# Kernel optimization log

Hardware: AMD Instinct MI355X
Metric: run time of the kernel (lower is better)

## Reference

```python
import jax, jax.numpy as jnp
import numpy as np

B, S, H, DH = 32, 512, 16, 64  # batch, seq_len (== dim_k), heads, head dim
DM = H * DH                     # d_model = 1024
DK = S                          # Linformer projection dim == seq_len (forced by Linear(dim_k, dim_k))


def setup_inputs() -> dict:
    key = jax.random.key(0)
    ks = jax.random.split(key, 16)
    sc = lambda fan_in: 1.0 / np.sqrt(fan_in)
    inp = {
        "query": jax.random.normal(ks[0], (B, S, DH), jnp.float32),
        "key":   jax.random.normal(ks[1], (B, S, DH), jnp.float32),
        "value": jax.random.normal(ks[2], (B, S, DH), jnp.float32),
        # per-head Q/K/V projections: torch Linear weight [out, in]
        "Wq": jax.random.uniform(ks[3], (H, DH, DH), jnp.float32, -sc(DH), sc(DH)),
        "bq": jax.random.uniform(ks[4], (H, DH), jnp.float32, -sc(DH), sc(DH)),
        "Wk": jax.random.uniform(ks[5], (H, DH, DH), jnp.float32, -sc(DH), sc(DH)),
        "bk": jax.random.uniform(ks[6], (H, DH), jnp.float32, -sc(DH), sc(DH)),
        "Wv": jax.random.uniform(ks[7], (H, DH, DH), jnp.float32, -sc(DH), sc(DH)),
        "bv": jax.random.uniform(ks[8], (H, DH), jnp.float32, -sc(DH), sc(DH)),
        # shared (headwise) E/F projections along the sequence dim: Linear(dim_k, dim_k)
        "E_w": jax.random.uniform(ks[9],  (DK, DK), jnp.float32, -sc(DK), sc(DK)),
        "E_b": jax.random.uniform(ks[10], (DK,),    jnp.float32, -sc(DK), sc(DK)),
        "F_w": jax.random.uniform(ks[11], (DK, DK), jnp.float32, -sc(DK), sc(DK)),
        "F_b": jax.random.uniform(ks[12], (DK,),    jnp.float32, -sc(DK), sc(DK)),
        # output projection Linear(d_model, d_model)
        "out_w": jax.random.uniform(ks[13], (DM, DM), jnp.float32, -sc(DM), sc(DM)),
        "out_b": jax.random.uniform(ks[14], (DM,),    jnp.float32, -sc(DM), sc(DM)),
    }
    return inp


def reference(query, key, value, Wq, bq, Wk, bk, Wv, bv, E_w, E_b, F_w, F_b, out_w, out_b):
    # Per-head linear projections (torch Linear: x @ W.T + b), vectorized over heads
    Q = jnp.einsum('bsd,hed->bhse', query, Wq) + bq[None, :, None, :]   # [B,H,S,DH]
    K = jnp.einsum('bsd,hed->bhse', key,   Wk) + bk[None, :, None, :]
    V = jnp.einsum('bsd,hed->bhse', value, Wv) + bv[None, :, None, :]

    # E projection along seq dim: K.permute -> [B,H,DH,S]; Linear(S,S) -> [B,H,DH,T]
    KE = jnp.einsum('bhsd,ts->bhdt', K, E_w) + E_b[None, None, None, :]  # [B,H,DH,T]
    # F projection along seq dim, then permute back: [B,H,T,DH]
    VF = jnp.einsum('bhsd,ts->bhtd', V, F_w) + F_b[None, None, :, None]  # [B,H,T,DH]

    scale = 1.0 / jnp.sqrt(jnp.float32(DH))  # scale uses d_head (K.size(-1) pre-permute)
    scores = jnp.einsum('bhsd,bhdt->bhst', Q, KE) * scale                # [B,H,S,T]
    attn = jax.nn.softmax(scores, axis=-1)                               # [B,H,S,T]
    head_out = jnp.einsum('bhst,bhtd->bhsd', attn, VF)                   # [B,H,S,DH]

    # concat heads on last dim: [B,S,H*DH]
    mha = head_out.transpose(0, 2, 1, 3).reshape(B, S, DM)
    mha_out = mha @ out_w.T + out_b                                      # [B,S,DM]
    return mha_out, attn
```

## Files before the change

kernel.cpp:

```cpp
#include <hip/hip_runtime.h>
#include <math.h>

#define B_  32
#define S_  512
#define H_  16
#define DH_ 64
#define DM_ 1024
#define T_  512

#define NBHSD (B_*H_*S_*DH_)
#define OFF_ATTN ((size_t)B_*S_*DM_)

__global__ __launch_bounds__(256)
void qkv_proj_kernel(const float* __restrict__ q_in, const float* __restrict__ k_in,
                     const float* __restrict__ v_in,
                     const float* __restrict__ Wq, const float* __restrict__ bq,
                     const float* __restrict__ Wk, const float* __restrict__ bk,
                     const float* __restrict__ Wv, const float* __restrict__ bv,
                     float* __restrict__ Qo, float* __restrict__ Ko, float* __restrict__ Vo)
{
    const int stile = blockIdx.x;
    const int h     = blockIdx.y;
    const int which = blockIdx.z / B_;
    const int b     = blockIdx.z % B_;

    const float* xin; const float* W; const float* bias; float* out;
    if (which == 0)      { xin = q_in; W = Wq; bias = bq; out = Qo; }
    else if (which == 1) { xin = k_in; W = Wk; bias = bk; out = Ko; }
    else                 { xin = v_in; W = Wv; bias = bv; out = Vo; }

    __shared__ float sA[32*68];
    __shared__ float sW[32*68];

    const int tid = threadIdx.x;
    const int dg = tid & 15;
    const int tg = tid >> 4;
    const int s0 = stile * 64;

    float acc[4][4];
    #pragma unroll
    for (int i=0;i<4;i++)
        #pragma unroll
        for (int j=0;j<4;j++) acc[i][j]=0.f;

    for (int dc = 0; dc < 64; dc += 32) {
        __syncthreads();
        for (int idx = tid; idx < 64*32; idx += 256) {
            int s = idx >> 5, d = idx & 31;
            sA[d*68 + s] = xin[((size_t)b*S_ + s0 + s)*DH_ + dc + d];
        }
        for (int idx = tid; idx < 64*32; idx += 256) {
            int e = idx >> 5, d = idx & 31;
            sW[d*68 + e] = W[(size_t)h*DH_*DH_ + (size_t)e*DH_ + dc + d];
        }
        __syncthreads();
        #pragma unroll
        for (int kk = 0; kk < 32; kk++) {
            const float4 a4 = *(const float4*)&sA[kk*68 + tg*4];
            const float4 w4 = *(const float4*)&sW[kk*68 + dg*4];
            const float a[4] = {a4.x,a4.y,a4.z,a4.w};
            const float w[4] = {w4.x,w4.y,w4.z,w4.w};
            #pragma unroll
            for (int i=0;i<4;i++)
                #pragma unroll
                for (int j=0;j<4;j++)
                    acc[i][j] = fmaf(a[i], w[j], acc[i][j]);
        }
    }

    const float4 bv4 = *(const float4*)&bias[h*DH_ + dg*4];
    const float bb[4] = {bv4.x,bv4.y,bv4.z,bv4.w};
    #pragma unroll
    for (int i=0;i<4;i++) {
        int s = s0 + tg*4 + i;
        float4 o;
        o.x = acc[i][0]+bb[0]; o.y = acc[i][1]+bb[1];
        o.z = acc[i][2]+bb[2]; o.w = acc[i][3]+bb[3];
        *(float4*)&out[(((size_t)b*H_ + h)*S_ + s)*DH_ + dg*4] = o;
    }
}

__global__ __launch_bounds__(256)
void gemm128x64_kernel(const float* __restrict__ A, long a_bh_stride, int K,
                       const float* __restrict__ X, long x_bh_stride,
                       const float* __restrict__ bias,
                       float* __restrict__ Y, long y_b_stride, long y_h_stride,
                       int y_row_stride)
{
    const int mtile = blockIdx.x;
    const int bh    = blockIdx.y;

    const float* Ab = A + (long)bh * a_bh_stride + (long)mtile*128*K;
    const float* Xb = X + (long)bh * x_bh_stride;

    __shared__ float sA[32*132];
    __shared__ float sX[32*72];

    const int tid = threadIdx.x;
    const int mg = tid >> 3;
    const int dg = tid & 7;
    const int mg4 = mg << 2;
    const int dg4 = dg << 2;

    float acc[4][8];
    #pragma unroll
    for (int i=0;i<4;i++)
        #pragma unroll
        for (int j=0;j<8;j++) acc[i][j]=0.f;

    for (int kc = 0; kc < K; kc += 32) {
        __syncthreads();
        #pragma unroll
        for (int w = 0; w < 4; w++) {
            int idx = tid + w*256;
            int m = idx >> 3, k4 = idx & 7;
            float4 v = *(const float4*)&Ab[(long)m*K + kc + k4*4];
            int col = (((m >> 2) ^ k4) << 2) + (m & 3);
            sA[(k4*4+0)*132 + col] = v.x;
            sA[(k4*4+1)*132 + col] = v.y;
            sA[(k4*4+2)*132 + col] = v.z;
            sA[(k4*4+3)*132 + col] = v.w;
        }
        #pragma unroll
        for (int w = 0; w < 2; w++) {
            int idx = tid + w*256;
            int k = idx >> 4, d4 = idx & 15;
            *(float4*)&sX[k*72 + d4*4] = *(const float4*)&Xb[(long)(kc+k)*64 + d4*4];
        }
        __syncthreads();
        #pragma unroll
        for (int kk = 0; kk < 32; kk++) {
            const int sm = mg4 ^ ((kk >> 2) << 2);
            const float4 a4 = *(const float4*)&sA[kk*132 + sm];
            const float4 x0 = *(const float4*)&sX[kk*72 + dg4];
            const float4 x1 = *(const float4*)&sX[kk*72 + 32 + dg4];
            const float a[4] = {a4.x,a4.y,a4.z,a4.w};
            const float x[8] = {x0.x,x0.y,x0.z,x0.w,x1.x,x1.y,x1.z,x1.w};
            #pragma unroll
            for (int i=0;i<4;i++)
                #pragma unroll
                for (int j=0;j<8;j++)
                    acc[i][j] = fmaf(a[i], x[j], acc[i][j]);
        }
    }

    const long ybase = (long)(bh >> 4)*y_b_stride + (long)(bh & 15)*y_h_stride
                     + (long)mtile*128*y_row_stride;
    #pragma unroll
    for (int i=0;i<4;i++) {
        int m = mg4 + i;
        float bval = bias ? bias[mtile*128 + m] : 0.f;
        float4 o0, o1;
        o0.x = acc[i][0]+bval; o0.y = acc[i][1]+bval;
        o0.z = acc[i][2]+bval; o0.w = acc[i][3]+bval;
        o1.x = acc[i][4]+bval; o1.y = acc[i][5]+bval;
        o1.z = acc[i][6]+bval; o1.w = acc[i][7]+bval;
        *(float4*)&Y[ybase + (long)m*y_row_stride + dg4]      = o0;
        *(float4*)&Y[ybase + (long)m*y_row_stride + 32 + dg4] = o1;
    }
}

__global__ __launch_bounds__(256)
void attn_softmax_kernel(const float* __restrict__ Q, const float* __restrict__ KEt,
                         float* __restrict__ attnOut)
{
    const int stile = blockIdx.x;
    const int bh    = blockIdx.y;

    __shared__ float sQt[64*36];
    __shared__ float sKt[64*132];

    const int tid = threadIdx.x;
    const int sq  = tid >> 5;
    const int tq  = tid & 31;
    const int tq4 = tq << 2;
    const int s0  = stile * 32;

    #pragma unroll
    for (int w = 0; w < 2; w++) {
        int idx = tid + w*256;
        int s = idx >> 4, d4 = idx & 15;
        float4 v = *(const float4*)&Q[((size_t)bh*S_ + s0 + s)*DH_ + d4*4];
        sQt[(d4*4+0)*36 + s] = v.x * 0.125f;
        sQt[(d4*4+1)*36 + s] = v.y * 0.125f;
        sQt[(d4*4+2)*36 + s] = v.z * 0.125f;
        sQt[(d4*4+3)*36 + s] = v.w * 0.125f;
    }

    float p[4][4][4];

    #pragma unroll
    for (int c = 0; c < 4; c++) {
        __syncthreads();
        #pragma unroll
        for (int w = 0; w < 8; w++) {
            int idx = tid + w*256;
            int t = idx >> 4, d4 = idx & 15;
            float4 v = *(const float4*)&KEt[((size_t)bh*T_ + c*128 + t)*DH_ + d4*4];
            int col = (((t >> 2) ^ d4) << 2) + (t & 3);
            sKt[(d4*4+0)*132 + col] = v.x;
            sKt[(d4*4+1)*132 + col] = v.y;
            sKt[(d4*4+2)*132 + col] = v.z;
            sKt[(d4*4+3)*132 + col] = v.w;
        }
        __syncthreads();

        #pragma unroll
        for (int i=0;i<4;i++)
            #pragma unroll
            for (int j=0;j<4;j++) p[c][i][j] = 0.f;

        #pragma unroll
        for (int kk = 0; kk < 64; kk++) {
            const float4 q4 = *(const float4*)&sQt[kk*36 + sq*4];
            const int st = tq4 ^ ((kk >> 2) << 2);
            const float4 k4 = *(const float4*)&sKt[kk*132 + st];
            const float q[4] = {q4.x,q4.y,q4.z,q4.w};
            const float k[4] = {k4.x,k4.y,k4.z,k4.w};
            #pragma unroll
            for (int i=0;i<4;i++)
                #pragma unroll
                for (int j=0;j<4;j++)
                    p[c][i][j] = fmaf(q[i], k[j], p[c][i][j]);
        }
    }

    #pragma unroll
    for (int i = 0; i < 4; i++) {
        float m = -INFINITY;
        #pragma unroll
        for (int c = 0; c < 4; c++)
            #pragma unroll
            for (int j = 0; j < 4; j++) m = fmaxf(m, p[c][i][j]);
        #pragma unroll
        for (int off = 16; off >= 1; off >>= 1) m = fmaxf(m, __shfl_xor(m, off));

        float sum = 0.f;
        #pragma unroll
        for (int c = 0; c < 4; c++)
            #pragma unroll
            for (int j = 0; j < 4; j++) {
                p[c][i][j] = __expf(p[c][i][j] - m);
                sum += p[c][i][j];
            }
        #pragma unroll
        for (int off = 16; off >= 1; off >>= 1) sum += __shfl_xor(sum, off);
        const float inv = 1.f / sum;

        const size_t rowbase = ((size_t)bh*S_ + s0 + sq*4 + i)*T_;
        #pragma unroll
        for (int c = 0; c < 4; c++) {
            float4 o;
            o.x = p[c][i][0]*inv; o.y = p[c][i][1]*inv;
            o.z = p[c][i][2]*inv; o.w = p[c][i][3]*inv;
            *(float4*)&attnOut[rowbase + c*128 + tq4] = o;
        }
    }
}

__global__ __launch_bounds__(256)
void outproj_kernel(const float* __restrict__ MHA, const float* __restrict__ Wout,
                    const float* __restrict__ bout, float* __restrict__ Yout)
{
    const int i0 = blockIdx.x*128;
    const int n0 = blockIdx.y*128;

    __shared__ float sA[32*132];
    __shared__ float sW[32*132];

    const int tid = threadIdx.x;
    const int mg = tid >> 4;
    const int ng = tid & 15;
    const int mg4 = mg << 2;
    const int ng4 = ng << 2;

    float acc[8][8];
    #pragma unroll
    for (int i=0;i<8;i++)
        #pragma unroll
        for (int j=0;j<8;j++) acc[i][j]=0.f;

    for (int kc = 0; kc < DM_; kc += 32) {
        __syncthreads();
        #pragma unroll
        for (int w = 0; w < 4; w++) {
            int idx = tid + w*256;
            int m = idx >> 3, k4 = idx & 7;
            float4 v = *(const float4*)&MHA[(long)(i0 + m)*DM_ + kc + k4*4];
            int col = (((m >> 2) ^ k4) << 2) + (m & 3);
            sA[(k4*4+0)*132 + col] = v.x;
            sA[(k4*4+1)*132 + col] = v.y;
            sA[(k4*4+2)*132 + col] = v.z;
            sA[(k4*4+3)*132 + col] = v.w;
        }
        #pragma unroll
        for (int w = 0; w < 4; w++) {
            int idx = tid + w*256;
            int n = idx >> 3, k4 = idx & 7;
            float4 v = *(const float4*)&Wout[(long)(n0 + n)*DM_ + kc + k4*4];
            int col = (((n >> 2) ^ k4) << 2) + (n & 3);
            sW[(k4*4+0)*132 + col] = v.x;
            sW[(k4*4+1)*132 + col] = v.y;
            sW[(k4*4+2)*132 + col] = v.z;
            sW[(k4*4+3)*132 + col] = v.w;
        }
        __syncthreads();
        #pragma unroll
        for (int kk = 0; kk < 32; kk++) {
            const int c4 = (kk >> 2) << 2;
            const int sm = mg4 ^ c4;
            const int sn = ng4 ^ c4;
            const float4 a0 = *(const float4*)&sA[kk*132 + sm];
            const float4 a1 = *(const float4*)&sA[kk*132 + 64 + sm];
            const float4 b0 = *(const float4*)&sW[kk*132 + sn];
            const float4 b1 = *(const float4*)&sW[kk*132 + 64 + sn];
            const float a[8] = {a0.x,a0.y,a0.z,a0.w,a1.x,a1.y,a1.z,a1.w};
            const float b[8] = {b0.x,b0.y,b0.z,b0.w,b1.x,b1.y,b1.z,b1.w};
            #pragma unroll
            for (int i=0;i<8;i++)
                #pragma unroll
                for (int j=0;j<8;j++)
                    acc[i][j] = fmaf(a[i], b[j], acc[i][j]);
        }
    }

    const float4 bv0 = *(const float4*)&bout[n0 + ng4];
    const float4 bv1 = *(const float4*)&bout[n0 + 64 + ng4];
    const float bb[8] = {bv0.x,bv0.y,bv0.z,bv0.w,bv1.x,bv1.y,bv1.z,bv1.w};
    #pragma unroll
    for (int ih = 0; ih < 2; ih++)
        #pragma unroll
        for (int ii = 0; ii < 4; ii++) {
            const int ai = ih*4 + ii;
            const long row = (long)(i0 + ih*64 + mg4 + ii)*DM_ + n0;
            float4 o0, o1;
            o0.x = acc[ai][0]+bb[0]; o0.y = acc[ai][1]+bb[1];
            o0.z = acc[ai][2]+bb[2]; o0.w = acc[ai][3]+bb[3];
            o1.x = acc[ai][4]+bb[4]; o1.y = acc[ai][5]+bb[5];
            o1.z = acc[ai][6]+bb[6]; o1.w = acc[ai][7]+bb[7];
            *(float4*)&Yout[row + ng4]      = o0;
            *(float4*)&Yout[row + 64 + ng4] = o1;
        }
}

extern "C" void kernel_launch(void* const* d_in, const int* in_sizes, int n_in,
                              void* d_out, int out_size, void* d_ws, size_t ws_size,
                              hipStream_t stream)
{
    const float* query = (const float*)d_in[0];
    const float* key   = (const float*)d_in[1];
    const float* value = (const float*)d_in[2];
    const float* Wq    = (const float*)d_in[3];
    const float* bq    = (const float*)d_in[4];
    const float* Wk    = (const float*)d_in[5];
    const float* bk    = (const float*)d_in[6];
    const float* Wv    = (const float*)d_in[7];
    const float* bv    = (const float*)d_in[8];
    const float* E_w   = (const float*)d_in[9];
    const float* E_b   = (const float*)d_in[10];
    const float* F_w   = (const float*)d_in[11];
    const float* F_b   = (const float*)d_in[12];
    const float* out_w = (const float*)d_in[13];
    const float* out_b = (const float*)d_in[14];

    float* ws   = (float*)d_ws;
    float* Qb   = ws;
    float* Kb   = ws + (size_t)NBHSD;
    float* Vb   = ws + (size_t)2*NBHSD;
    float* KEt  = ws + (size_t)3*NBHSD;
    float* VF   = ws + (size_t)4*NBHSD;
    float* MHA  = Qb;

    float* mha_out = (float*)d_out;
    float* attn    = (float*)d_out + OFF_ATTN;

    qkv_proj_kernel<<<dim3(S_/64, H_, 3*B_), 256, 0, stream>>>(
        query, key, value, Wq, bq, Wk, bk, Wv, bv, Qb, Kb, Vb);

    gemm128x64_kernel<<<dim3(T_/128, B_*H_), 256, 0, stream>>>(
        E_w, 0, S_, Kb, (long)S_*DH_, E_b,
        KEt, (long)H_*T_*DH_, (long)T_*DH_, DH_);
    gemm128x64_kernel<<<dim3(T_/128, B_*H_), 256, 0, stream>>>(
        F_w, 0, S_, Vb, (long)S_*DH_, F_b,
        VF, (long)H_*T_*DH_, (long)T_*DH_, DH_);

    attn_softmax_kernel<<<dim3(S_/32, B_*H_), 256, 0, stream>>>(Qb, KEt, attn);

    gemm128x64_kernel<<<dim3(S_/128, B_*H_), 256, 0, stream>>>(
        attn, (long)S_*T_, T_, VF, (long)T_*DH_, nullptr,
        MHA, (long)S_*DM_, (long)DH_, DM_);

    outproj_kernel<<<dim3(B_*S_/128, DM_/128), 256, 0, stream>>>(
        MHA, out_w, out_b, mha_out);
}
```

Baseline: 2.114 ms.

## Run output projection on bf16 MFMA with hi/lo split-precision operands

```diff
diff --git a/kernel.cpp b/kernel.cpp
--- a/kernel.cpp
+++ b/kernel.cpp
@@ -10,6 +10,19 @@
 
 #define NBHSD (B_*H_*S_*DH_)
 #define OFF_ATTN ((size_t)B_*S_*DM_)
+
+typedef __attribute__((ext_vector_type(8))) short     bf16x8;
+typedef __attribute__((ext_vector_type(4))) float     f32x4;
+typedef __attribute__((ext_vector_type(8))) unsigned short u16x8;
+
+__device__ __forceinline__ unsigned short f2bf(float x) {
+    unsigned int u = __float_as_uint(x);
+    u = (u + 0x7FFFu + ((u >> 16) & 1u)) >> 16;
+    return (unsigned short)u;
+}
+__device__ __forceinline__ float bf2f(unsigned short h) {
+    return __uint_as_float(((unsigned int)h) << 16);
+}
 
 __global__ __launch_bounds__(256)
 void qkv_proj_kernel(const float* __restrict__ q_in, const float* __restrict__ k_in,
@@ -259,34 +272,37 @@
 }
 
 __global__ __launch_bounds__(256)
-void outproj_kernel(const float* __restrict__ MHA, const float* __restrict__ Wout,
-                    const float* __restrict__ bout, float* __restrict__ Yout)
-{
-    const int i0 = blockIdx.x*128;
-    const int n0 = blockIdx.y*128;
+void pv_bf16out_kernel(const float* __restrict__ A, const float* __restrict__ X,
+                       ushort* __restrict__ Yhi, ushort* __restrict__ Ylo)
+{
+    const int mtile = blockIdx.x;
+    const int bh    = blockIdx.y;
+
+    const float* Ab = A + (size_t)bh*S_*T_ + (size_t)mtile*128*T_;
+    const float* Xb = X + (size_t)bh*T_*DH_;
 
     __shared__ float sA[32*132];
-    __shared__ float sW[32*132];
+    __shared__ float sX[32*72];
 
     const int tid = threadIdx.x;
-    const int mg = tid >> 4;
-    const int ng = tid & 15;
+    const int mg = tid >> 3;
+    const int dg = tid & 7;
     const int mg4 = mg << 2;
-    const int ng4 = ng << 2;
-
-    float acc[8][8];
-    #pragma unroll
-    for (int i=0;i<8;i++)
+    const int dg4 = dg << 2;
+
+    float acc[4][8];
+    #pragma unroll
+    for (int i=0;i<4;i++)
         #pragma unroll
         for (int j=0;j<8;j++) acc[i][j]=0.f;
 
-    for (int kc = 0; kc < DM_; kc += 32) {
+    for (int kc = 0; kc < T_; kc += 32) {
         __syncthreads();
         #pragma unroll
         for (int w = 0; w < 4; w++) {
             int idx = tid + w*256;
             int m = idx >> 3, k4 = idx & 7;
-            float4 v = *(const float4*)&MHA[(long)(i0 + m)*DM_ + kc + k4*4];
+            float4 v = *(const float4*)&Ab[(long)m*T_ + kc + k4*4];
             int col = (((m >> 2) ^ k4) << 2) + (m & 3);
             sA[(k4*4+0)*132 + col] = v.x;
             sA[(k4*4+1)*132 + col] = v.y;
@@ -294,53 +310,151 @@
             sA[(k4*4+3)*132 + col] = v.w;
         }
         #pragma unroll
-        for (int w = 0; w < 4; w++) {
+        for (int w = 0; w < 2; w++) {
             int idx = tid + w*256;
-            int n = idx >> 3, k4 = idx & 7;
-            float4 v = *(const float4*)&Wout[(long)(n0 + n)*DM_ + kc + k4*4];
-            int col = (((n >> 2) ^ k4) << 2) + (n & 3);
-            sW[(k4*4+0)*132 + col] = v.x;
-            sW[(k4*4+1)*132 + col] = v.y;
-            sW[(k4*4+2)*132 + col] = v.z;
-            sW[(k4*4+3)*132 + col] = v.w;
+            int k = idx >> 4, d4 = idx & 15;
+            *(float4*)&sX[k*72 + d4*4] = *(const float4*)&Xb[(long)(kc+k)*64 + d4*4];
         }
         __syncthreads();
         #pragma unroll
         for (int kk = 0; kk < 32; kk++) {
-            const int c4 = (kk >> 2) << 2;
-            const int sm = mg4 ^ c4;
-            const int sn = ng4 ^ c4;
-            const float4 a0 = *(const float4*)&sA[kk*132 + sm];
-            const float4 a1 = *(const float4*)&sA[kk*132 + 64 + sm];
-            const float4 b0 = *(const float4*)&sW[kk*132 + sn];
-            const float4 b1 = *(const float4*)&sW[kk*132 + 64 + sn];
-            const float a[8] = {a0.x,a0.y,a0.z,a0.w,a1.x,a1.y,a1.z,a1.w};
-            const float b[8] = {b0.x,b0.y,b0.z,b0.w,b1.x,b1.y,b1.z,b1.w};
-            #pragma unroll
-            for (int i=0;i<8;i++)
+            const int sm = mg4 ^ ((kk >> 2) << 2);
+            const float4 a4 = *(const float4*)&sA[kk*132 + sm];
+            const float4 x0 = *(const float4*)&sX[kk*72 + dg4];
+            const float4 x1 = *(const float4*)&sX[kk*72 + 32 + dg4];
+            const float a[4] = {a4.x,a4.y,a4.z,a4.w};
+            const float x[8] = {x0.x,x0.y,x0.z,x0.w,x1.x,x1.y,x1.z,x1.w};
+            #pragma unroll
+            for (int i=0;i<4;i++)
                 #pragma unroll
                 for (int j=0;j<8;j++)
-                    acc[i][j] = fmaf(a[i], b[j], acc[i][j]);
-        }
-    }
-
-    const float4 bv0 = *(const float4*)&bout[n0 + ng4];
-    const float4 bv1 = *(const float4*)&bout[n0 + 64 + ng4];
-    const float bb[8] = {bv0.x,bv0.y,bv0.z,bv0.w,bv1.x,bv1.y,bv1.z,bv1.w};
-    #pragma unroll
-    for (int ih = 0; ih < 2; ih++)
-        #pragma unroll
-        for (int ii = 0; ii < 4; ii++) {
-            const int ai = ih*4 + ii;
-            const long row = (long)(i0 + ih*64 + mg4 + ii)*DM_ + n0;
-            float4 o0, o1;
-            o0.x = acc[ai][0]+bb[0]; o0.y = acc[ai][1]+bb[1];
-            o0.z = acc[ai][2]+bb[2]; o0.w = acc[ai][3]+bb[3];
-            o1.x = acc[ai][4]+bb[4]; o1.y = acc[ai][5]+bb[5];
-            o1.z = acc[ai][6]+bb[6]; o1.w = acc[ai][7]+bb[7];
-            *(float4*)&Yout[row + ng4]      = o0;
-            *(float4*)&Yout[row + 64 + ng4] = o1;
-        }
+                    acc[i][j] = fmaf(a[i], x[j], acc[i][j]);
+        }
+    }
+
+    const size_t ybase = (size_t)(bh >> 4)*S_*DM_ + (size_t)(bh & 15)*DH_
+                       + (size_t)mtile*128*DM_;
+    #pragma unroll
+    for (int i=0;i<4;i++) {
+        const int m = mg4 + i;
+        const size_t rb = ybase + (size_t)m*DM_;
+        ushort4 h0, l0, h1, l1;
+        h0.x = f2bf(acc[i][0]); l0.x = f2bf(acc[i][0] - bf2f(h0.x));
+        h0.y = f2bf(acc[i][1]); l0.y = f2bf(acc[i][1] - bf2f(h0.y));
+        h0.z = f2bf(acc[i][2]); l0.z = f2bf(acc[i][2] - bf2f(h0.z));
+        h0.w = f2bf(acc[i][3]); l0.w = f2bf(acc[i][3] - bf2f(h0.w));
+        h1.x = f2bf(acc[i][4]); l1.x = f2bf(acc[i][4] - bf2f(h1.x));
+        h1.y = f2bf(acc[i][5]); l1.y = f2bf(acc[i][5] - bf2f(h1.y));
+        h1.z = f2bf(acc[i][6]); l1.z = f2bf(acc[i][6] - bf2f(h1.z));
+        h1.w = f2bf(acc[i][7]); l1.w = f2bf(acc[i][7] - bf2f(h1.w));
+        *(ushort4*)&Yhi[rb + dg4]      = h0;
+        *(ushort4*)&Ylo[rb + dg4]      = l0;
+        *(ushort4*)&Yhi[rb + 32 + dg4] = h1;
+        *(ushort4*)&Ylo[rb + 32 + dg4] = l1;
+    }
+}
+
+__global__ __launch_bounds__(256)
+void wconv_kernel(const float* __restrict__ W, ushort* __restrict__ Whi,
+                  ushort* __restrict__ Wlo)
+{
+    const size_t i = ((size_t)blockIdx.x*256 + threadIdx.x)*4;
+    float4 v = *(const float4*)&W[i];
+    ushort4 h, l;
+    h.x = f2bf(v.x); l.x = f2bf(v.x - bf2f(h.x));
+    h.y = f2bf(v.y); l.y = f2bf(v.y - bf2f(h.y));
+    h.z = f2bf(v.z); l.z = f2bf(v.z - bf2f(h.z));
+    h.w = f2bf(v.w); l.w = f2bf(v.w - bf2f(h.w));
+    *(ushort4*)&Whi[i] = h;
+    *(ushort4*)&Wlo[i] = l;
+}
+
+__global__ __launch_bounds__(256)
+void outproj_mfma_kernel(const ushort* __restrict__ Ahi, const ushort* __restrict__ Alo,
+                         const ushort* __restrict__ Bhi, const ushort* __restrict__ Blo,
+                         const float* __restrict__ bout, float* __restrict__ Yout)
+{
+    const int i0 = blockIdx.x * 128;
+    const int n0 = blockIdx.y * 128;
+
+    __shared__ __align__(16) ushort sAh[128*40];
+    __shared__ __align__(16) ushort sAl[128*40];
+    __shared__ __align__(16) ushort sBh[128*40];
+    __shared__ __align__(16) ushort sBl[128*40];
+
+    const int tid  = threadIdx.x;
+    const int lane = tid & 63;
+    const int wave = tid >> 6;
+    const int wm   = wave >> 1;
+    const int wn   = wave & 1;
+    const int l15  = lane & 15;
+    const int l4   = lane >> 4;
+
+    const int srow = tid >> 2;
+    const int koff = (tid & 3) * 8;
+
+    f32x4 acc[4][4];
+    #pragma unroll
+    for (int a=0;a<4;a++)
+        #pragma unroll
+        for (int b=0;b<4;b++)
+            acc[a][b] = (f32x4){0.f,0.f,0.f,0.f};
+
+    for (int kc = 0; kc < DM_; kc += 32) {
+        __syncthreads();
+        #pragma unroll
+        for (int p = 0; p < 2; p++) {
+            const int r = p*64 + srow;
+            const size_t gi = (size_t)(i0 + r)*DM_ + kc + koff;
+            const size_t gn = (size_t)(n0 + r)*DM_ + kc + koff;
+            *(u16x8*)&sAh[r*40 + koff] = *(const u16x8*)&Ahi[gi];
+            *(u16x8*)&sAl[r*40 + koff] = *(const u16x8*)&Alo[gi];
+            *(u16x8*)&sBh[r*40 + koff] = *(const u16x8*)&Bhi[gn];
+            *(u16x8*)&sBl[r*40 + koff] = *(const u16x8*)&Blo[gn];
+        }
+        __syncthreads();
+
+        bf16x8 ah[4], al[4], bh[4], bl[4];
+        #pragma unroll
+        for (int q = 0; q < 4; q++) {
+            ah[q] = *(const bf16x8*)&sAh[(wm*64 + q*16 + l15)*40 + l4*8];
+            al[q] = *(const bf16x8*)&sAl[(wm*64 + q*16 + l15)*40 + l4*8];
+            bh[q] = *(const bf16x8*)&sBh[(wn*64 + q*16 + l15)*40 + l4*8];
+            bl[q] = *(const bf16x8*)&sBl[(wn*64 + q*16 + l15)*40 + l4*8];
+        }
+        #pragma unroll
+        for (int mb=0; mb<4; mb++)
+            #pragma unroll
+            for (int nb=0; nb<4; nb++)
+                acc[mb][nb] = __builtin_amdgcn_mfma_f32_16x16x32_bf16(
+                                  ah[mb], bh[nb], acc[mb][nb], 0, 0, 0);
+        #pragma unroll
+        for (int mb=0; mb<4; mb++)
+            #pragma unroll
+            for (int nb=0; nb<4; nb++)
+                acc[mb][nb] = __builtin_amdgcn_mfma_f32_16x16x32_bf16(
+                                  ah[mb], bl[nb], acc[mb][nb], 0, 0, 0);
+        #pragma unroll
+        for (int mb=0; mb<4; mb++)
+            #pragma unroll
+            for (int nb=0; nb<4; nb++)
+                acc[mb][nb] = __builtin_amdgcn_mfma_f32_16x16x32_bf16(
+                                  al[mb], bh[nb], acc[mb][nb], 0, 0, 0);
+    }
+
+    #pragma unroll
+    for (int nb = 0; nb < 4; nb++) {
+        const int n = n0 + wn*64 + nb*16 + l15;
+        const float bias = bout[n];
+        #pragma unroll
+        for (int mb = 0; mb < 4; mb++) {
+            #pragma unroll
+            for (int r = 0; r < 4; r++) {
+                const int row = i0 + wm*64 + mb*16 + l4*4 + r;
+                Yout[(size_t)row*DM_ + n] = acc[mb][nb][r] + bias;
+            }
+        }
+    }
 }
 
 extern "C" void kernel_launch(void* const* d_in, const int* in_sizes, int n_in,
@@ -369,7 +483,11 @@
     float* Vb   = ws + (size_t)2*NBHSD;
     float* KEt  = ws + (size_t)3*NBHSD;
     float* VF   = ws + (size_t)4*NBHSD;
-    float* MHA  = Qb;
+
+    ushort* MHAhi = (ushort*)Qb;
+    ushort* MHAlo = MHAhi + (size_t)NBHSD;
+    ushort* Whi   = (ushort*)Kb;
+    ushort* Wlo   = Whi + (size_t)DM_*DM_;
 
     float* mha_out = (float*)d_out;
     float* attn    = (float*)d_out + OFF_ATTN;
@@ -384,12 +502,13 @@
         F_w, 0, S_, Vb, (long)S_*DH_, F_b,
         VF, (long)H_*T_*DH_, (long)T_*DH_, DH_);
 
+    wconv_kernel<<<dim3(DM_*DM_/1024), 256, 0, stream>>>(out_w, Whi, Wlo);
+
     attn_softmax_kernel<<<dim3(S_/32, B_*H_), 256, 0, stream>>>(Qb, KEt, attn);
 
-    gemm128x64_kernel<<<dim3(S_/128, B_*H_), 256, 0, stream>>>(
-        attn, (long)S_*T_, T_, VF, (long)T_*DH_, nullptr,
-        MHA, (long)S_*DM_, (long)DH_, DM_);
-
-    outproj_kernel<<<dim3(B_*S_/128, DM_/128), 256, 0, stream>>>(
-        MHA, out_w, out_b, mha_out);
-}
+    pv_bf16out_kernel<<<dim3(S_/128, B_*H_), 256, 0, stream>>>(
+        attn, VF, MHAhi, MHAlo);
+
+    outproj_mfma_kernel<<<dim3(B_*S_/128, DM_/128), 256, 0, stream>>>(
+        MHAhi, MHAlo, Whi, Wlo, out_b, mha_out);
+}
```

Result: faster. 1.818 ms (-14.0%).
